# Kernel tuning notes

Measured on AMD Instinct MI355X. Metric: run time of the kernel, lower is better.

## Reference

```python
import jax, jax.numpy as jnp
import numpy as np

N_HEADS = 16


def setup_inputs() -> dict:
    key = jax.random.key(0)
    ks = jax.random.split(key, 8)
    B, S, D = 4, 2048, 1024
    scale = 1.0 / np.sqrt(D)
    return {
        "x": jax.random.normal(ks[0], (B, S, D), dtype=jnp.float32),
        "Wq": jax.random.normal(ks[1], (D, D), dtype=jnp.float32) * scale,
        "bq": jax.random.normal(ks[2], (D,), dtype=jnp.float32) * 0.01,
        "Wk": jax.random.normal(ks[3], (D, D), dtype=jnp.float32) * scale,
        "bk": jax.random.normal(ks[4], (D,), dtype=jnp.float32) * 0.01,
        "Wv": jax.random.normal(ks[5], (D, D), dtype=jnp.float32) * scale,
        "bv": jax.random.normal(ks[6], (D,), dtype=jnp.float32) * 0.01,
        "mask": jax.random.randint(ks[7], (B, S), 0, 2, dtype=jnp.int32),
    }


def reference(x, Wq, bq, Wk, bk, Wv, bv, mask):
    B, S, D = x.shape
    H = N_HEADS
    W = D // H
    # QKV projections (Linear with weight stored input-major: y = x @ W + b)
    q = (x @ Wq + bq).reshape(B, S, H, W).transpose(0, 2, 1, 3)  # (B,H,S,W)
    k = (x @ Wk + bk).reshape(B, S, H, W).transpose(0, 2, 1, 3)
    v = (x @ Wv + bv).reshape(B, S, H, W).transpose(0, 2, 1, 3)
    # scaled dot-product scores: (B,H,S,S)
    scores = jnp.einsum("bhsw,bhtw->bhst", q, k) / jnp.sqrt(jnp.asarray(W, x.dtype))
    # mask==1 means masked (subtract large constant), per original code
    scores = scores - 10000.0 * mask[:, None, None, :].astype(x.dtype)
    attn = jax.nn.softmax(scores, axis=-1)  # dropout p=0 -> identity
    h = jnp.einsum("bhst,bhtw->bhsw", attn, v)  # (B,H,S,W)
    h = h.transpose(0, 2, 1, 3).reshape(B, S, D)
    return h
```

## Files before the change

kernel.cpp:

```cpp
#include <hip/hip_runtime.h>
#include <math.h>

#define B_NUM 4
#define S_LEN 2048
#define D_DIM 1024
#define H_NUM 16
#define W_DIM 64

typedef float4 f4;
typedef _Float16 f16;
typedef f16 f16x8 __attribute__((ext_vector_type(8)));
typedef f16 f16x4 __attribute__((ext_vector_type(4)));
typedef float floatx4 __attribute__((ext_vector_type(4)));

#define GLOAD_LDS16(gp, lp)                                                     \
    __builtin_amdgcn_global_load_lds(                                           \
        (const __attribute__((address_space(1))) void*)(gp),                    \
        (__attribute__((address_space(3))) void*)(lp), 16, 0, 0)

__global__ __launch_bounds__(256) void compact_kernel(
    const int* __restrict__ mask, short* __restrict__ fwdmap,
    int* __restrict__ cnt)
{
    __shared__ int sc[256];
    const int b   = blockIdx.x;
    const int tid = threadIdx.x;
    const int t0  = tid * 8;

#pragma unroll
    for (int j = 0; j < 8; ++j) fwdmap[b * S_LEN + t0 + j] = 0;

    int kept[8], c = 0;
#pragma unroll
    for (int j = 0; j < 8; ++j) {
        kept[j] = (mask[b * S_LEN + t0 + j] == 0);
        c += kept[j];
    }
    sc[tid] = c;
    __syncthreads();
    for (int off = 1; off < 256; off <<= 1) {
        int add = (tid >= off) ? sc[tid - off] : 0;
        __syncthreads();
        sc[tid] += add;
        __syncthreads();
    }
    int base = sc[tid] - c;
#pragma unroll
    for (int j = 0; j < 8; ++j)
        if (kept[j]) fwdmap[b * S_LEN + (base++)] = (short)(t0 + j);
    if (tid == 255) {
        cnt[b * 4 + 0] = sc[255];
        cnt[b * 4 + 1] = (sc[255] + 63) & ~63;
        cnt[b * 4 + 2] = (sc[255] + 127) & ~127;
    }
}

__global__ __launch_bounds__(256) void cast_x_kernel(
    const float* __restrict__ x, f16* __restrict__ x16)
{
    const size_t i = (size_t)blockIdx.x * 256 + threadIdx.x;
    f4 t = *(const f4*)&x[i * 4];
    f16x4 o;
    o[0] = (f16)t.x; o[1] = (f16)t.y; o[2] = (f16)t.z; o[3] = (f16)t.w;
    *(f16x4*)&x16[i * 4] = o;
}

__global__ __launch_bounds__(256) void transpose_w_kernel(
    const float* __restrict__ Wq, const float* __restrict__ Wk,
    const float* __restrict__ Wv, f16* __restrict__ wt16)
{
    __shared__ float ts[64][68];

    const int tid = threadIdx.x;
    const int k0 = blockIdx.x * 64;
    const int n0 = blockIdx.y * 64;
    const float* Wsel = (blockIdx.z == 0) ? Wq : (blockIdx.z == 1) ? Wk : Wv;
    f16* outp = wt16 + (size_t)blockIdx.z * D_DIM * D_DIM;

    const int r  = tid >> 4;
    const int c4 = (tid & 15) * 4;
#pragma unroll
    for (int i = 0; i < 4; ++i) {
        f4 t = *(const f4*)&Wsel[(size_t)(k0 + r + i * 16) * D_DIM + n0 + c4];
        *(f4*)&ts[r + i * 16][c4] = t;
    }
    __syncthreads();
#pragma unroll
    for (int i = 0; i < 4; ++i) {
        int idx = tid + i * 256;
        int nl = idx >> 4;
        int k4 = (idx & 15) * 4;
        f16x4 o;
#pragma unroll
        for (int j = 0; j < 4; ++j) o[j] = (f16)ts[k4 + j][nl];
        *(f16x4*)&outp[(size_t)(n0 + nl) * D_DIM + k0 + k4] = o;
    }
}

__global__ __launch_bounds__(256) void qkv_mfma_kernel(
    const f16* __restrict__ x16, const f16* __restrict__ wt16,
    const float* __restrict__ bq, const float* __restrict__ bk,
    const float* __restrict__ bv, const short* __restrict__ fwdmap,
    const int* __restrict__ cnt,
    f16* __restrict__ Qo, f16* __restrict__ Ko, f16* __restrict__ Vo)
{
    __shared__ f16 As[128 * 64];
    __shared__ f16 Bs[128 * 64];

    const int tid  = threadIdx.x;
    const int lane = tid & 63;
    const int wid  = tid >> 6;
    const int lx   = lane & 15;
    const int quad = lane >> 4;
    const int wm   = wid >> 1;
    const int wn   = wid & 1;

    const int r0    = blockIdx.y * 128;
    const int nt    = blockIdx.x;
    const int midx  = nt >> 3;
    const int c0    = (nt & 7) * 128;
    const int bB    = r0 >> 11;
    const int r0loc = r0 & (S_LEN - 1);

    if (midx > 0 && r0loc >= cnt[bB * 4 + 2]) return;

    const f16* Bg = wt16 + (size_t)midx * D_DIM * D_DIM + (size_t)c0 * D_DIM;

    const int srow = lane >> 3;
    const int scw  = ((lane & 7) ^ srow) * 8;

    int arows[4];
#pragma unroll
    for (int it = 0; it < 4; ++it) {
        int rl = (wid * 4 + it) * 8 + srow;
        arows[it] = (midx == 0)
            ? (r0 + rl)
            : (bB * S_LEN + (int)fwdmap[bB * S_LEN + r0loc + rl]);
    }

    floatx4 acc[4][4];
#pragma unroll
    for (int a = 0; a < 4; ++a)
#pragma unroll
        for (int b = 0; b < 4; ++b) { acc[a][b][0]=0.f; acc[a][b][1]=0.f; acc[a][b][2]=0.f; acc[a][b][3]=0.f; }

    for (int k0 = 0; k0 < D_DIM; k0 += 64) {
        __syncthreads();
#pragma unroll
        for (int it = 0; it < 4; ++it) {
            int chunk = wid * 4 + it;
            GLOAD_LDS16(&x16[(size_t)arows[it] * D_DIM + k0 + scw], &As[chunk * 512]);
            GLOAD_LDS16(&Bg[(size_t)(chunk * 8 + srow) * D_DIM + k0 + scw], &Bs[chunk * 512]);
        }
        __syncthreads();

#pragma unroll
        for (int kh = 0; kh < 2; ++kh) {
            const int csw = ((kh * 4 + quad) ^ (lx & 7)) * 8;
            f16x8 af[4], bf[4];
#pragma unroll
            for (int tm = 0; tm < 4; ++tm)
                af[tm] = *(const f16x8*)&As[(wm * 64 + tm * 16 + lx) * 64 + csw];
#pragma unroll
            for (int tn = 0; tn < 4; ++tn)
                bf[tn] = *(const f16x8*)&Bs[(wn * 64 + tn * 16 + lx) * 64 + csw];
#pragma unroll
            for (int tm = 0; tm < 4; ++tm)
#pragma unroll
                for (int tn = 0; tn < 4; ++tn)
                    acc[tm][tn] = __builtin_amdgcn_mfma_f32_16x16x32_f16(
                        af[tm], bf[tn], acc[tm][tn], 0, 0, 0);
        }
    }

    const float* bp = (midx == 0) ? bq : (midx == 1) ? bk : bv;
    float bias[4];
#pragma unroll
    for (int tn = 0; tn < 4; ++tn)
        bias[tn] = bp[c0 + wn * 64 + tn * 16 + lx];

    if (midx == 0) {
#pragma unroll
        for (int tm = 0; tm < 4; ++tm) {
            int s = r0loc + wm * 64 + tm * 16 + quad * 4;
#pragma unroll
            for (int tn = 0; tn < 4; ++tn) {
                int gc = c0 + wn * 64 + tn * 16 + lx;
                int h = gc >> 6, w = gc & 63;
                size_t base = (((size_t)(bB * H_NUM + h)) * S_LEN + s) * W_DIM + w;
#pragma unroll
                for (int rr = 0; rr < 4; ++rr)
                    Qo[base + (size_t)rr * W_DIM] =
                        (f16)((acc[tm][tn][rr] + bias[tn]) * 0.125f);
            }
        }
    } else if (midx == 1) {
#pragma unroll
        for (int tm = 0; tm < 4; ++tm) {
            int jc = r0loc + wm * 64 + tm * 16 + quad * 4;
#pragma unroll
            for (int tn = 0; tn < 4; ++tn) {
                int gc = c0 + wn * 64 + tn * 16 + lx;
                int h = gc >> 6, w = gc & 63;
                size_t base = (((size_t)(bB * H_NUM + h)) * S_LEN + jc) * W_DIM + w;
#pragma unroll
                for (int rr = 0; rr < 4; ++rr)
                    Ko[base + (size_t)rr * W_DIM] = (f16)(acc[tm][tn][rr] + bias[tn]);
            }
        }
    } else {
#pragma unroll
        for (int tm = 0; tm < 4; ++tm) {
            int jc = r0loc + wm * 64 + tm * 16 + quad * 4;
#pragma unroll
            for (int tn = 0; tn < 4; ++tn) {
                int gc = c0 + wn * 64 + tn * 16 + lx;
                int h = gc >> 6, w = gc & 63;
                f16x4 v;
#pragma unroll
                for (int rr = 0; rr < 4; ++rr) v[rr] = (f16)(acc[tm][tn][rr] + bias[tn]);
                *(f16x4*)&Vo[(((size_t)(bB * H_NUM + h)) * W_DIM + w) * S_LEN + jc] = v;
            }
        }
    }
}

#define LSTR 72

__global__ __launch_bounds__(256) void attn_kernel(
    const f16* __restrict__ Q, const f16* __restrict__ Kc,
    const f16* __restrict__ Vct, const int* __restrict__ cnt,
    float* __restrict__ out)
{
    __shared__ f16 Ks[64][LSTR];
    __shared__ f16 Vs[64][LSTR];

    const int tid  = threadIdx.x;
    const int lane = tid & 63;
    const int wid  = tid >> 6;
    const int lx   = lane & 15;
    const int quad = lane >> 4;
    const int qt = blockIdx.x, h = blockIdx.y, bb = blockIdx.z;

    const int count = cnt[bb * 4 + 0];
    const int scp   = cnt[bb * 4 + 1];

    const size_t hoff = ((size_t)(bb * H_NUM + h)) * S_LEN * W_DIM;
    const f16* Qg = Q + hoff + (size_t)qt * 128 * W_DIM;
    const f16* Kg = Kc + hoff;
    const f16* Vg = Vct + hoff;

    f16x8 qb[2][2];
#pragma unroll
    for (int u = 0; u < 2; ++u) {
        int qrow = u * 64 + wid * 16 + lx;
        qb[u][0] = *(const f16x8*)&Qg[(size_t)qrow * W_DIM + quad * 8];
        qb[u][1] = *(const f16x8*)&Qg[(size_t)qrow * W_DIM + 32 + quad * 8];
    }

    floatx4 o[2][4];
    float lsum[2] = {0.f, 0.f};
#pragma unroll
    for (int u = 0; u < 2; ++u)
#pragma unroll
        for (int wb = 0; wb < 4; ++wb) { o[u][wb][0]=0.f; o[u][wb][1]=0.f; o[u][wb][2]=0.f; o[u][wb][3]=0.f; }

    for (int k0 = 0; k0 < scp; k0 += 64) {
        __syncthreads();
#pragma unroll
        for (int it = 0; it < 2; ++it) {
            int idx = tid + it * 256;
            int row = idx >> 3, c8 = (idx & 7) * 8;
            *(f16x8*)&Ks[row][c8] = *(const f16x8*)&Kg[(size_t)(k0 + row) * W_DIM + c8];
            *(f16x8*)&Vs[row][c8] = *(const f16x8*)&Vg[(size_t)row * S_LEN + k0 + c8];
        }
        __syncthreads();

        const bool tail = (k0 + 64 > count);

        f16x4 pb[2][4];
#pragma unroll
        for (int n = 0; n < 4; ++n) {
            f16x8 ka0 = *(const f16x8*)&Ks[n * 16 + lx][quad * 8];
            f16x8 ka1 = *(const f16x8*)&Ks[n * 16 + lx][32 + quad * 8];
            const int kb = k0 + n * 16 + quad * 4;
#pragma unroll
            for (int u = 0; u < 2; ++u) {
                floatx4 s; s[0]=0.f; s[1]=0.f; s[2]=0.f; s[3]=0.f;
                s = __builtin_amdgcn_mfma_f32_16x16x32_f16(ka0, qb[u][0], s, 0, 0, 0);
                s = __builtin_amdgcn_mfma_f32_16x16x32_f16(ka1, qb[u][1], s, 0, 0, 0);
                float p[4], ls = 0.f;
                if (tail) {
#pragma unroll
                    for (int r = 0; r < 4; ++r) {
                        float sv = (kb + r < count) ? s[r] : -1.0e4f;
                        p[r] = __expf(sv); ls += p[r];
                    }
                } else {
#pragma unroll
                    for (int r = 0; r < 4; ++r) { p[r] = __expf(s[r]); ls += p[r]; }
                }
                lsum[u] += ls;
#pragma unroll
                for (int r = 0; r < 4; ++r) pb[u][n][r] = (f16)p[r];
            }
        }

#pragma unroll
        for (int wb = 0; wb < 4; ++wb) {
#pragma unroll
            for (int n = 0; n < 4; ++n) {
                f16x4 va = *(const f16x4*)&Vs[wb * 16 + lx][n * 16 + quad * 4];
#pragma unroll
                for (int u = 0; u < 2; ++u)
                    o[u][wb] = __builtin_amdgcn_mfma_f32_16x16x16f16(va, pb[u][n], o[u][wb], 0, 0, 0);
            }
        }
    }

#pragma unroll
    for (int u = 0; u < 2; ++u) {
        float ls = lsum[u];
        ls += __shfl_xor(ls, 16);
        ls += __shfl_xor(ls, 32);
        const float rl = 1.0f / ls;
        const int q = qt * 128 + u * 64 + wid * 16 + lx;
        const size_t base = ((size_t)bb * S_LEN + q) * D_DIM + h * W_DIM;
#pragma unroll
        for (int wb = 0; wb < 4; ++wb) {
            f4 r;
            r.x = o[u][wb][0] * rl;
            r.y = o[u][wb][1] * rl;
            r.z = o[u][wb][2] * rl;
            r.w = o[u][wb][3] * rl;
            *(f4*)&out[base + wb * 16 + quad * 4] = r;
        }
    }
}

extern "C" void kernel_launch(void* const* d_in, const int* in_sizes, int n_in,
                              void* d_out, int out_size, void* d_ws, size_t ws_size,
                              hipStream_t stream)
{
    const float* x    = (const float*)d_in[0];
    const float* Wq   = (const float*)d_in[1];
    const float* bq   = (const float*)d_in[2];
    const float* Wk   = (const float*)d_in[3];
    const float* bk   = (const float*)d_in[4];
    const float* Wv   = (const float*)d_in[5];
    const float* bv   = (const float*)d_in[6];
    const int*   mask = (const int*)d_in[7];
    float* out = (float*)d_out;

    const size_t per = (size_t)B_NUM * H_NUM * S_LEN * W_DIM;
    f16*   Q      = (f16*)d_ws;
    f16*   Kc     = Q + per;
    f16*   Vct    = Kc + per;
    f16*   x16    = Vct + per;
    f16*   wt16   = x16 + (size_t)(B_NUM * S_LEN) * D_DIM;
    int*   cnt    = (int*)(wt16 + (size_t)3 * D_DIM * D_DIM);
    short* fwdmap = (short*)(cnt + 4 * B_NUM);

    compact_kernel<<<B_NUM, 256, 0, stream>>>(mask, fwdmap, cnt);
    cast_x_kernel<<<(B_NUM * S_LEN * D_DIM) / 1024, 256, 0, stream>>>(x, x16);
    transpose_w_kernel<<<dim3(16, 16, 3), 256, 0, stream>>>(Wq, Wk, Wv, wt16);
    qkv_mfma_kernel<<<dim3(24, 64), 256, 0, stream>>>(
        x16, wt16, bq, bk, bv, fwdmap, cnt, Q, Kc, Vct);
    attn_kernel<<<dim3(S_LEN / 128, H_NUM, B_NUM), 256, 0, stream>>>(
        Q, Kc, Vct, cnt, out);
}
```

Measured before the change: 221.2 us.

## Rewrite QKV GEMM as 256x256 tile, 8-wave, double-buffered pipelined MFMA kernel

```diff
diff --git a/kernel.cpp b/kernel.cpp
--- a/kernel.cpp
+++ b/kernel.cpp
@@ -6,6 +6,7 @@
 #define D_DIM 1024
 #define H_NUM 16
 #define W_DIM 64
+#define NT    (D_DIM / 64)
 
 typedef float4 f4;
 typedef _Float16 f16;
@@ -52,6 +53,7 @@
         cnt[b * 4 + 0] = sc[255];
         cnt[b * 4 + 1] = (sc[255] + 63) & ~63;
         cnt[b * 4 + 2] = (sc[255] + 127) & ~127;
+        cnt[b * 4 + 3] = (sc[255] + 255) & ~255;
     }
 }
 
@@ -97,128 +99,187 @@
     }
 }
 
-__global__ __launch_bounds__(256) void qkv_mfma_kernel(
+
+#define STAGE_A(BUF, P, KT) do {                                                \
+    GLOAD_LDS16(asrc[P][0] + (size_t)(KT) * 64, &lds[BUF][0][(P)*128 + wid*8][0]);        \
+    GLOAD_LDS16(asrc[P][1] + (size_t)(KT) * 64, &lds[BUF][0][(P)*128 + 64 + wid*8][0]);   \
+} while (0)
+
+#define STAGE_B(BUF, P, KT) do {                                                \
+    GLOAD_LDS16(bsrc[P][0] + (size_t)(KT) * 64, &lds[BUF][1][(P)*128 + wid*8][0]);        \
+    GLOAD_LDS16(bsrc[P][1] + (size_t)(KT) * 64, &lds[BUF][1][(P)*128 + 64 + wid*8][0]);   \
+} while (0)
+
+#define LDS_A(CUR, MABS, KH) \
+    (*(const f16x8*)&lds[CUR][0][(MABS)*32 + wm16 + lx][(((KH)*4 + quad) ^ lx7) * 8])
+#define LDS_B(CUR, NABS, KH) \
+    (*(const f16x8*)&lds[CUR][1][(NABS)*64 + wn16 + lx][(((KH)*4 + quad) ^ lx7) * 8])
+
+#define MFMA_PH(MB, NB) do {                                                    \
+    __builtin_amdgcn_s_setprio(1);                                              \
+    _Pragma("unroll") for (int m_ = 0; m_ < 4; ++m_)                            \
+    _Pragma("unroll") for (int n_ = 0; n_ < 2; ++n_)                            \
+    _Pragma("unroll") for (int kh_ = 0; kh_ < 2; ++kh_)                         \
+        acc[(MB) + m_][(NB) + n_] = __builtin_amdgcn_mfma_f32_16x16x32_f16(     \
+            af[m_][kh_], bf[(NB) + n_][kh_], acc[(MB) + m_][(NB) + n_], 0, 0, 0);\
+    __builtin_amdgcn_s_setprio(0);                                              \
+} while (0)
+
+#define VMCNT8()  asm volatile("s_waitcnt vmcnt(8)" ::: "memory")
+#define LGKM0()   do { asm volatile("s_waitcnt lgkmcnt(0)" ::: "memory");       \
+                       __builtin_amdgcn_sched_barrier(0); } while (0)
+#define BAR()     __builtin_amdgcn_s_barrier()
+
+#define QKV_TILE(T, CUR, NXT) do {                                              \
+                                            \
+    _Pragma("unroll") for (int m_ = 0; m_ < 4; ++m_) {                          \
+        af[m_][0] = LDS_A(CUR, m_, 0); af[m_][1] = LDS_A(CUR, m_, 1); }         \
+    _Pragma("unroll") for (int n_ = 0; n_ < 2; ++n_) {                          \
+        bf[n_][0] = LDS_B(CUR, n_, 0); bf[n_][1] = LDS_B(CUR, n_, 1); }         \
+    { int kt = ((T) + 1 < NT) ? (T) + 1 : NT - 1; STAGE_A(NXT, 1, kt); }        \
+    VMCNT8(); BAR(); LGKM0();                                                   \
+    MFMA_PH(0, 0);                                                              \
+    BAR();                                                                      \
+                                            \
+    _Pragma("unroll") for (int n_ = 0; n_ < 2; ++n_) {                          \
+        bf[2 + n_][0] = LDS_B(CUR, 2 + n_, 0); bf[2 + n_][1] = LDS_B(CUR, 2 + n_, 1); } \
+    { int kt = ((T) + 2 < NT) ? (T) + 2 : NT - 1; STAGE_A(CUR, 0, kt); }        \
+    VMCNT8(); BAR(); LGKM0();                                                   \
+    MFMA_PH(0, 2);                                                              \
+    BAR();                                                                      \
+                                            \
+    _Pragma("unroll") for (int m_ = 0; m_ < 4; ++m_) {                          \
+        af[m_][0] = LDS_A(CUR, 4 + m_, 0); af[m_][1] = LDS_A(CUR, 4 + m_, 1); } \
+    { int kt = ((T) + 2 < NT) ? (T) + 2 : NT - 1; STAGE_B(CUR, 0, kt); }        \
+    VMCNT8(); BAR(); LGKM0();                                                   \
+    MFMA_PH(4, 0);                                                              \
+    BAR();                                                                      \
+             \
+    { int kt = ((T) + 2 < NT) ? (T) + 2 : NT - 1; STAGE_B(CUR, 1, kt); }        \
+    VMCNT8(); BAR();                                                            \
+    __builtin_amdgcn_sched_barrier(0);                                          \
+    MFMA_PH(4, 2);                                                              \
+    BAR();                                                                      \
+} while (0)
+
+__global__ __launch_bounds__(512, 2) void qkv_mfma_kernel(
     const f16* __restrict__ x16, const f16* __restrict__ wt16,
     const float* __restrict__ bq, const float* __restrict__ bk,
     const float* __restrict__ bv, const short* __restrict__ fwdmap,
     const int* __restrict__ cnt,
     f16* __restrict__ Qo, f16* __restrict__ Ko, f16* __restrict__ Vo)
 {
-    __shared__ f16 As[128 * 64];
-    __shared__ f16 Bs[128 * 64];
+    __shared__ f16 lds[2][2][256][64];
 
     const int tid  = threadIdx.x;
     const int lane = tid & 63;
     const int wid  = tid >> 6;
     const int lx   = lane & 15;
     const int quad = lane >> 4;
-    const int wm   = wid >> 1;
-    const int wn   = wid & 1;
-
-    const int r0    = blockIdx.y * 128;
-    const int nt    = blockIdx.x;
-    const int midx  = nt >> 3;
-    const int c0    = (nt & 7) * 128;
+    const int lx7  = lx & 7;
+    const int wm   = wid >> 2;
+    const int wn   = wid & 3;
+    const int wm16 = wm * 16;
+    const int wn16 = wn * 16;
+
+    const int mtile = blockIdx.x;
+    const int nt    = blockIdx.y;
+    const int midx  = nt >> 2;
+    const int c0    = (nt & 3) * 256;
+    const int r0    = mtile * 256;
     const int bB    = r0 >> 11;
     const int r0loc = r0 & (S_LEN - 1);
 
-    if (midx > 0 && r0loc >= cnt[bB * 4 + 2]) return;
-
-    const f16* Bg = wt16 + (size_t)midx * D_DIM * D_DIM + (size_t)c0 * D_DIM;
-
-    const int srow = lane >> 3;
-    const int scw  = ((lane & 7) ^ srow) * 8;
-
-    int arows[4];
-#pragma unroll
-    for (int it = 0; it < 4; ++it) {
-        int rl = (wid * 4 + it) * 8 + srow;
-        arows[it] = (midx == 0)
-            ? (r0 + rl)
-            : (bB * S_LEN + (int)fwdmap[bB * S_LEN + r0loc + rl]);
-    }
-
-    floatx4 acc[4][4];
-#pragma unroll
-    for (int a = 0; a < 4; ++a)
-#pragma unroll
-        for (int b = 0; b < 4; ++b) { acc[a][b][0]=0.f; acc[a][b][1]=0.f; acc[a][b][2]=0.f; acc[a][b][3]=0.f; }
-
-    for (int k0 = 0; k0 < D_DIM; k0 += 64) {
-        __syncthreads();
-#pragma unroll
-        for (int it = 0; it < 4; ++it) {
-            int chunk = wid * 4 + it;
-            GLOAD_LDS16(&x16[(size_t)arows[it] * D_DIM + k0 + scw], &As[chunk * 512]);
-            GLOAD_LDS16(&Bg[(size_t)(chunk * 8 + srow) * D_DIM + k0 + scw], &Bs[chunk * 512]);
-        }
-        __syncthreads();
-
-#pragma unroll
-        for (int kh = 0; kh < 2; ++kh) {
-            const int csw = ((kh * 4 + quad) ^ (lx & 7)) * 8;
-            f16x8 af[4], bf[4];
-#pragma unroll
-            for (int tm = 0; tm < 4; ++tm)
-                af[tm] = *(const f16x8*)&As[(wm * 64 + tm * 16 + lx) * 64 + csw];
-#pragma unroll
-            for (int tn = 0; tn < 4; ++tn)
-                bf[tn] = *(const f16x8*)&Bs[(wn * 64 + tn * 16 + lx) * 64 + csw];
-#pragma unroll
-            for (int tm = 0; tm < 4; ++tm)
-#pragma unroll
-                for (int tn = 0; tn < 4; ++tn)
-                    acc[tm][tn] = __builtin_amdgcn_mfma_f32_16x16x32_f16(
-                        af[tm], bf[tn], acc[tm][tn], 0, 0, 0);
-        }
-    }
+    if (midx > 0 && r0loc >= cnt[bB * 4 + 3]) return;
+
+    const int srow8 = lane >> 3;
+    const int scw   = ((lane & 7) ^ srow8) * 8;
+
+    const f16* asrc[2][2];
+    const f16* bsrc[2][2];
+#pragma unroll
+    for (int p = 0; p < 2; ++p)
+#pragma unroll
+        for (int r = 0; r < 2; ++r) {
+            int lrow = p * 128 + r * 64 + wid * 8 + srow8;
+            int ar = (midx == 0)
+                ? (r0 + lrow)
+                : (bB * S_LEN + (int)fwdmap[bB * S_LEN + r0loc + lrow]);
+            asrc[p][r] = x16 + (size_t)ar * D_DIM + scw;
+            bsrc[p][r] = wt16 + (size_t)midx * D_DIM * D_DIM
+                              + (size_t)(c0 + lrow) * D_DIM + scw;
+        }
+
+    floatx4 acc[8][4];
+#pragma unroll
+    for (int m = 0; m < 8; ++m)
+#pragma unroll
+        for (int n = 0; n < 4; ++n) {
+            acc[m][n][0] = 0.f; acc[m][n][1] = 0.f;
+            acc[m][n][2] = 0.f; acc[m][n][3] = 0.f;
+        }
+
+    f16x8 af[4][2];
+    f16x8 bf[4][2];
+
+    STAGE_A(0, 0, 0); STAGE_A(0, 1, 0); STAGE_B(0, 0, 0); STAGE_B(0, 1, 0);
+    STAGE_A(1, 0, 1); STAGE_B(1, 0, 1); STAGE_B(1, 1, 1);
+    asm volatile("s_waitcnt vmcnt(0)" ::: "memory");
+    BAR();
+
+    for (int tt = 0; tt < NT; tt += 2) {
+        QKV_TILE(tt,     0, 1);
+        QKV_TILE(tt + 1, 1, 0);
+    }
+
+    asm volatile("s_waitcnt vmcnt(0)" ::: "memory");
 
     const float* bp = (midx == 0) ? bq : (midx == 1) ? bk : bv;
     float bias[4];
 #pragma unroll
-    for (int tn = 0; tn < 4; ++tn)
-        bias[tn] = bp[c0 + wn * 64 + tn * 16 + lx];
+    for (int n = 0; n < 4; ++n)
+        bias[n] = bp[c0 + n * 64 + wn16 + lx];
 
     if (midx == 0) {
 #pragma unroll
-        for (int tm = 0; tm < 4; ++tm) {
-            int s = r0loc + wm * 64 + tm * 16 + quad * 4;
-#pragma unroll
-            for (int tn = 0; tn < 4; ++tn) {
-                int gc = c0 + wn * 64 + tn * 16 + lx;
+        for (int m = 0; m < 8; ++m) {
+            int s = r0loc + m * 32 + wm16 + quad * 4;
+#pragma unroll
+            for (int n = 0; n < 4; ++n) {
+                int gc = c0 + n * 64 + wn16 + lx;
                 int h = gc >> 6, w = gc & 63;
                 size_t base = (((size_t)(bB * H_NUM + h)) * S_LEN + s) * W_DIM + w;
 #pragma unroll
                 for (int rr = 0; rr < 4; ++rr)
                     Qo[base + (size_t)rr * W_DIM] =
-                        (f16)((acc[tm][tn][rr] + bias[tn]) * 0.125f);
+                        (f16)((acc[m][n][rr] + bias[n]) * 0.125f);
             }
         }
     } else if (midx == 1) {
 #pragma unroll
-        for (int tm = 0; tm < 4; ++tm) {
-            int jc = r0loc + wm * 64 + tm * 16 + quad * 4;
-#pragma unroll
-            for (int tn = 0; tn < 4; ++tn) {
-                int gc = c0 + wn * 64 + tn * 16 + lx;
+        for (int m = 0; m < 8; ++m) {
+            int jc = r0loc + m * 32 + wm16 + quad * 4;
+#pragma unroll
+            for (int n = 0; n < 4; ++n) {
+                int gc = c0 + n * 64 + wn16 + lx;
                 int h = gc >> 6, w = gc & 63;
                 size_t base = (((size_t)(bB * H_NUM + h)) * S_LEN + jc) * W_DIM + w;
 #pragma unroll
                 for (int rr = 0; rr < 4; ++rr)
-                    Ko[base + (size_t)rr * W_DIM] = (f16)(acc[tm][tn][rr] + bias[tn]);
+                    Ko[base + (size_t)rr * W_DIM] = (f16)(acc[m][n][rr] + bias[n]);
             }
         }
     } else {
 #pragma unroll
-        for (int tm = 0; tm < 4; ++tm) {
-            int jc = r0loc + wm * 64 + tm * 16 + quad * 4;
-#pragma unroll
-            for (int tn = 0; tn < 4; ++tn) {
-                int gc = c0 + wn * 64 + tn * 16 + lx;
+        for (int m = 0; m < 8; ++m) {
+            int jc = r0loc + m * 32 + wm16 + quad * 4;
+#pragma unroll
+            for (int n = 0; n < 4; ++n) {
+                int gc = c0 + n * 64 + wn16 + lx;
                 int h = gc >> 6, w = gc & 63;
                 f16x4 v;
 #pragma unroll
-                for (int rr = 0; rr < 4; ++rr) v[rr] = (f16)(acc[tm][tn][rr] + bias[tn]);
+                for (int rr = 0; rr < 4; ++rr) v[rr] = (f16)(acc[m][n][rr] + bias[n]);
                 *(f16x4*)&Vo[(((size_t)(bB * H_NUM + h)) * W_DIM + w) * S_LEN + jc] = v;
             }
         }
@@ -364,7 +425,7 @@
     compact_kernel<<<B_NUM, 256, 0, stream>>>(mask, fwdmap, cnt);
     cast_x_kernel<<<(B_NUM * S_LEN * D_DIM) / 1024, 256, 0, stream>>>(x, x16);
     transpose_w_kernel<<<dim3(16, 16, 3), 256, 0, stream>>>(Wq, Wk, Wv, wt16);
-    qkv_mfma_kernel<<<dim3(24, 64), 256, 0, stream>>>(
+    qkv_mfma_kernel<<<dim3(32, 12), 512, 0, stream>>>(
         x16, wt16, bq, bk, bv, fwdmap, cnt, Q, Kc, Vct);
     attn_kernel<<<dim3(S_LEN / 128, H_NUM, B_NUM), 256, 0, stream>>>(
         Q, Kc, Vct, cnt, out);
```

Result: no change. 225.6 us (+2.0%).

## Merge prep kernels into one launch and read K/V directly from global in attention

Applied to the files above, without the earlier changes.

```diff
diff --git a/kernel.cpp b/kernel.cpp
--- a/kernel.cpp
+++ b/kernel.cpp
@@ -18,82 +18,83 @@
         (const __attribute__((address_space(1))) void*)(gp),                    \
         (__attribute__((address_space(3))) void*)(lp), 16, 0, 0)
 
-__global__ __launch_bounds__(256) void compact_kernel(
+#define TR_BLOCKS   768
+#define CAST_BLOCKS 8192
+
+__global__ __launch_bounds__(256) void prep_kernel(
     const int* __restrict__ mask, short* __restrict__ fwdmap,
-    int* __restrict__ cnt)
-{
-    __shared__ int sc[256];
-    const int b   = blockIdx.x;
-    const int tid = threadIdx.x;
-    const int t0  = tid * 8;
-
-#pragma unroll
-    for (int j = 0; j < 8; ++j) fwdmap[b * S_LEN + t0 + j] = 0;
-
-    int kept[8], c = 0;
-#pragma unroll
-    for (int j = 0; j < 8; ++j) {
-        kept[j] = (mask[b * S_LEN + t0 + j] == 0);
-        c += kept[j];
-    }
-    sc[tid] = c;
-    __syncthreads();
-    for (int off = 1; off < 256; off <<= 1) {
-        int add = (tid >= off) ? sc[tid - off] : 0;
-        __syncthreads();
-        sc[tid] += add;
-        __syncthreads();
-    }
-    int base = sc[tid] - c;
-#pragma unroll
-    for (int j = 0; j < 8; ++j)
-        if (kept[j]) fwdmap[b * S_LEN + (base++)] = (short)(t0 + j);
-    if (tid == 255) {
-        cnt[b * 4 + 0] = sc[255];
-        cnt[b * 4 + 1] = (sc[255] + 63) & ~63;
-        cnt[b * 4 + 2] = (sc[255] + 127) & ~127;
-    }
-}
-
-__global__ __launch_bounds__(256) void cast_x_kernel(
+    int* __restrict__ cnt,
+    const float* __restrict__ Wq, const float* __restrict__ Wk,
+    const float* __restrict__ Wv, f16* __restrict__ wt16,
     const float* __restrict__ x, f16* __restrict__ x16)
 {
-    const size_t i = (size_t)blockIdx.x * 256 + threadIdx.x;
-    f4 t = *(const f4*)&x[i * 4];
-    f16x4 o;
-    o[0] = (f16)t.x; o[1] = (f16)t.y; o[2] = (f16)t.z; o[3] = (f16)t.w;
-    *(f16x4*)&x16[i * 4] = o;
-}
-
-__global__ __launch_bounds__(256) void transpose_w_kernel(
-    const float* __restrict__ Wq, const float* __restrict__ Wk,
-    const float* __restrict__ Wv, f16* __restrict__ wt16)
-{
-    __shared__ float ts[64][68];
-
+    __shared__ __align__(16) char smraw[64 * 68 * 4];
+    const int bx  = blockIdx.x;
     const int tid = threadIdx.x;
-    const int k0 = blockIdx.x * 64;
-    const int n0 = blockIdx.y * 64;
-    const float* Wsel = (blockIdx.z == 0) ? Wq : (blockIdx.z == 1) ? Wk : Wv;
-    f16* outp = wt16 + (size_t)blockIdx.z * D_DIM * D_DIM;
-
-    const int r  = tid >> 4;
-    const int c4 = (tid & 15) * 4;
-#pragma unroll
-    for (int i = 0; i < 4; ++i) {
-        f4 t = *(const f4*)&Wsel[(size_t)(k0 + r + i * 16) * D_DIM + n0 + c4];
-        *(f4*)&ts[r + i * 16][c4] = t;
-    }
-    __syncthreads();
-#pragma unroll
-    for (int i = 0; i < 4; ++i) {
-        int idx = tid + i * 256;
-        int nl = idx >> 4;
-        int k4 = (idx & 15) * 4;
+
+    if (bx < 4) {
+        int* sc = (int*)smraw;
+        const int b  = bx;
+        const int t0 = tid * 8;
+#pragma unroll
+        for (int j = 0; j < 8; ++j) fwdmap[b * S_LEN + t0 + j] = 0;
+        int kept[8], c = 0;
+#pragma unroll
+        for (int j = 0; j < 8; ++j) {
+            kept[j] = (mask[b * S_LEN + t0 + j] == 0);
+            c += kept[j];
+        }
+        sc[tid] = c;
+        __syncthreads();
+        for (int off = 1; off < 256; off <<= 1) {
+            int add = (tid >= off) ? sc[tid - off] : 0;
+            __syncthreads();
+            sc[tid] += add;
+            __syncthreads();
+        }
+        int base = sc[tid] - c;
+#pragma unroll
+        for (int j = 0; j < 8; ++j)
+            if (kept[j]) fwdmap[b * S_LEN + (base++)] = (short)(t0 + j);
+        if (tid == 255) {
+            cnt[b * 4 + 0] = sc[255];
+            cnt[b * 4 + 1] = (sc[255] + 63) & ~63;
+            cnt[b * 4 + 2] = (sc[255] + 127) & ~127;
+            cnt[b * 4 + 3] = (sc[255] + 255) & ~255;
+        }
+    } else if (bx < 4 + TR_BLOCKS) {
+        float (*ts)[68] = (float(*)[68])smraw;
+        const int idx = bx - 4;
+        const int k0 = (idx & 15) * 64;
+        const int n0 = ((idx >> 4) & 15) * 64;
+        const int z  = idx >> 8;
+        const float* Wsel = (z == 0) ? Wq : (z == 1) ? Wk : Wv;
+        f16* outp = wt16 + (size_t)z * D_DIM * D_DIM;
+
+        const int r  = tid >> 4;
+        const int c4 = (tid & 15) * 4;
+#pragma unroll
+        for (int i = 0; i < 4; ++i) {
+            f4 t = *(const f4*)&Wsel[(size_t)(k0 + r + i * 16) * D_DIM + n0 + c4];
+            *(f4*)&ts[r + i * 16][c4] = t;
+        }
+        __syncthreads();
+#pragma unroll
+        for (int i = 0; i < 4; ++i) {
+            int id2 = tid + i * 256;
+            int nl = id2 >> 4;
+            int k4 = (id2 & 15) * 4;
+            f16x4 o;
+#pragma unroll
+            for (int j = 0; j < 4; ++j) o[j] = (f16)ts[k4 + j][nl];
+            *(f16x4*)&outp[(size_t)(n0 + nl) * D_DIM + k0 + k4] = o;
+        }
+    } else {
+        const size_t i = (size_t)(bx - 4 - TR_BLOCKS) * 256 + tid;
+        f4 t = *(const f4*)&x[i * 4];
         f16x4 o;
-#pragma unroll
-        for (int j = 0; j < 4; ++j) o[j] = (f16)ts[k4 + j][nl];
-        *(f16x4*)&outp[(size_t)(n0 + nl) * D_DIM + k0 + k4] = o;
+        o[0] = (f16)t.x; o[1] = (f16)t.y; o[2] = (f16)t.z; o[3] = (f16)t.w;
+        *(f16x4*)&x16[i * 4] = o;
     }
 }
 
@@ -225,16 +226,11 @@
     }
 }
 
-#define LSTR 72
-
 __global__ __launch_bounds__(256) void attn_kernel(
     const f16* __restrict__ Q, const f16* __restrict__ Kc,
     const f16* __restrict__ Vct, const int* __restrict__ cnt,
     float* __restrict__ out)
 {
-    __shared__ f16 Ks[64][LSTR];
-    __shared__ f16 Vs[64][LSTR];
-
     const int tid  = threadIdx.x;
     const int lane = tid & 63;
     const int wid  = tid >> 6;
@@ -266,23 +262,14 @@
         for (int wb = 0; wb < 4; ++wb) { o[u][wb][0]=0.f; o[u][wb][1]=0.f; o[u][wb][2]=0.f; o[u][wb][3]=0.f; }
 
     for (int k0 = 0; k0 < scp; k0 += 64) {
-        __syncthreads();
-#pragma unroll
-        for (int it = 0; it < 2; ++it) {
-            int idx = tid + it * 256;
-            int row = idx >> 3, c8 = (idx & 7) * 8;
-            *(f16x8*)&Ks[row][c8] = *(const f16x8*)&Kg[(size_t)(k0 + row) * W_DIM + c8];
-            *(f16x8*)&Vs[row][c8] = *(const f16x8*)&Vg[(size_t)row * S_LEN + k0 + c8];
-        }
-        __syncthreads();
-
         const bool tail = (k0 + 64 > count);
 
         f16x4 pb[2][4];
 #pragma unroll
         for (int n = 0; n < 4; ++n) {
-            f16x8 ka0 = *(const f16x8*)&Ks[n * 16 + lx][quad * 8];
-            f16x8 ka1 = *(const f16x8*)&Ks[n * 16 + lx][32 + quad * 8];
+            const int krow = k0 + n * 16 + lx;
+            f16x8 ka0 = *(const f16x8*)&Kg[(size_t)krow * W_DIM + quad * 8];
+            f16x8 ka1 = *(const f16x8*)&Kg[(size_t)krow * W_DIM + 32 + quad * 8];
             const int kb = k0 + n * 16 + quad * 4;
 #pragma unroll
             for (int u = 0; u < 2; ++u) {
@@ -310,7 +297,8 @@
         for (int wb = 0; wb < 4; ++wb) {
 #pragma unroll
             for (int n = 0; n < 4; ++n) {
-                f16x4 va = *(const f16x4*)&Vs[wb * 16 + lx][n * 16 + quad * 4];
+                f16x4 va = *(const f16x4*)&Vg[(size_t)(wb * 16 + lx) * S_LEN
+                                              + k0 + n * 16 + quad * 4];
 #pragma unroll
                 for (int u = 0; u < 2; ++u)
                     o[u][wb] = __builtin_amdgcn_mfma_f32_16x16x16f16(va, pb[u][n], o[u][wb], 0, 0, 0);
@@ -361,9 +349,8 @@
     int*   cnt    = (int*)(wt16 + (size_t)3 * D_DIM * D_DIM);
     short* fwdmap = (short*)(cnt + 4 * B_NUM);
 
-    compact_kernel<<<B_NUM, 256, 0, stream>>>(mask, fwdmap, cnt);
-    cast_x_kernel<<<(B_NUM * S_LEN * D_DIM) / 1024, 256, 0, stream>>>(x, x16);
-    transpose_w_kernel<<<dim3(16, 16, 3), 256, 0, stream>>>(Wq, Wk, Wv, wt16);
+    prep_kernel<<<4 + TR_BLOCKS + CAST_BLOCKS, 256, 0, stream>>>(
+        mask, fwdmap, cnt, Wq, Wk, Wv, wt16, x, x16);
     qkv_mfma_kernel<<<dim3(24, 64), 256, 0, stream>>>(
         x16, wt16, bq, bk, bv, fwdmap, cnt, Q, Kc, Vct);
     attn_kernel<<<dim3(S_LEN / 128, H_NUM, B_NUM), 256, 0, stream>>>(
```

Measured after the change: 364.9 us. +65.0%, slower.
